# Performance work log

Measured on AMD Instinct MI355X. Metric: run time of the kernel, lower is better.

The kernel has to match this reference:

```python
import jax, jax.numpy as jnp
import numpy as np

N = 100000
E = 3200000
IN_F = 256
OUT_F = 64
ALPHA = 0.2  # LeakyReLU negative slope


def setup_inputs() -> dict:
    key = jax.random.key(0)
    k1, k2, k3, k4 = jax.random.split(key, 4)
    adj = jax.random.randint(k1, (2, E), 0, N, dtype=jnp.int64)
    x = jax.random.normal(k2, (N, IN_F), dtype=jnp.float32)
    # xavier-normal-ish scales
    W_fc = jax.random.normal(k3, (OUT_F, IN_F), dtype=jnp.float32) * (1.414 * np.sqrt(2.0 / (IN_F + OUT_F)))
    b_fc = jnp.zeros((OUT_F,), dtype=jnp.float32)
    a = jax.random.normal(k4, (1, 2 * OUT_F), dtype=jnp.float32) * (1.414 * np.sqrt(2.0 / (1 + 2 * OUT_F)))
    return {"adj": adj, "x": x, "W_fc": W_fc, "b_fc": b_fc, "a": a}


def reference(adj, x, W_fc, b_fc, a):
    src = adj[0]  # [E]
    dst = adj[1]  # [E]
    h = x @ W_fc.T + b_fc                       # [N, OUT_F]
    a1, a2 = a[0, :OUT_F], a[0, OUT_F:]         # split of attention vector
    # e = leakyrelu(a . [h_src || h_dst]) computed without materializing concat
    s1 = h @ a1                                  # [N]
    s2 = h @ a2                                  # [N]
    e = s1[src] + s2[dst]                        # [E]
    e = jnp.where(e > 0, e, ALPHA * e)           # LeakyReLU
    # dgl edge_softmax: softmax over edges grouped by destination node
    m = jax.ops.segment_max(e, dst, num_segments=N)     # [N]
    ex = jnp.exp(e - m[dst])                             # [E]
    denom = jax.ops.segment_sum(ex, dst, num_segments=N) # [N]
    att = ex / denom[dst]                                # [E]
    # SparseTensor(row=src, col=dst, value=att) @ h -> out[src] += att * h[dst]
    h_prime = jax.ops.segment_sum(att[:, None] * h[dst], src, num_segments=N)  # [N, OUT_F]
    return jax.nn.elu(h_prime)  # concat=True branch
```

## Files before the change

### kernel.cpp

```cpp
#include <hip/hip_runtime.h>
#include <math.h>

#define N_NODES 100000
#define N_EDGES 3200000
#define IN_F 256
#define OUT_F 64
#define LRELU_ALPHA 0.2f
#define NBKT 782
#define CAP 4480

typedef unsigned short u16;
typedef __attribute__((ext_vector_type(8))) short short8;
typedef __attribute__((ext_vector_type(4))) float floatx4;

__device__ inline u16 f2bf(float f) {
  unsigned u = __float_as_uint(f);
  u += 0x7FFFu + ((u >> 16) & 1u);
  return (u16)(u >> 16);
}
__device__ inline float bf2f(u16 h) {
  return __uint_as_float(((unsigned)h) << 16);
}

__global__ __launch_bounds__(256) void k_prep(const float* __restrict__ W,
                                              u16* __restrict__ Wbf,
                                              int* __restrict__ sfill,
                                              int* __restrict__ dfill) {
  if (blockIdx.x < 64) {
    int i = blockIdx.x * 256 + threadIdx.x;
    Wbf[i] = f2bf(W[i]);
  } else {
    for (int i = threadIdx.x; i < NBKT; i += 256) {
      sfill[i] = 0;
      dfill[i] = 0;
    }
  }
}

__global__ __launch_bounds__(256) void k_linear(
    const float* __restrict__ x, const u16* __restrict__ Wbf,
    const float* __restrict__ b, const float* __restrict__ a,
    u16* __restrict__ hbf, float* __restrict__ s1, float* __restrict__ s2) {
  __shared__ u16 Wlds[64 * 264];

  const int t = threadIdx.x;
#pragma unroll
  for (int p = 0; p < 8; p++) {
    int c = p * 256 + t;
    int row = c >> 5;
    int kc = (c & 31) * 8;
    *(short8*)&Wlds[row * 264 + kc] = *(const short8*)&Wbf[row * 256 + kc];
  }
  __syncthreads();

  const int w = t >> 6;
  const int lane = t & 63;
  const int col = lane & 15;
  const int q = lane >> 4;
  const int m0 = blockIdx.x * 64 + w * 16;

  floatx4 acc[4];
#pragma unroll
  for (int nt = 0; nt < 4; nt++) acc[nt] = (floatx4){0.f, 0.f, 0.f, 0.f};

  int mrow = m0 + col;
  if (mrow > N_NODES - 1) mrow = N_NODES - 1;
  const float* xrow = x + (size_t)mrow * IN_F + q * 8;

#pragma unroll
  for (int kk = 0; kk < 8; kk++) {
    float4 f0 = *(const float4*)(xrow + kk * 32);
    float4 f1 = *(const float4*)(xrow + kk * 32 + 4);
    short8 af;
    af[0] = (short)f2bf(f0.x);
    af[1] = (short)f2bf(f0.y);
    af[2] = (short)f2bf(f0.z);
    af[3] = (short)f2bf(f0.w);
    af[4] = (short)f2bf(f1.x);
    af[5] = (short)f2bf(f1.y);
    af[6] = (short)f2bf(f1.z);
    af[7] = (short)f2bf(f1.w);
#pragma unroll
    for (int nt = 0; nt < 4; nt++) {
      short8 bfr = *(const short8*)&Wlds[(nt * 16 + col) * 264 + kk * 32 + q * 8];
      acc[nt] = __builtin_amdgcn_mfma_f32_16x16x32_bf16(af, bfr, acc[nt], 0, 0, 0);
    }
  }

  float bv[4], a1v[4], a2v[4];
#pragma unroll
  for (int nt = 0; nt < 4; nt++) {
    bv[nt] = b[nt * 16 + col];
    a1v[nt] = a[nt * 16 + col];
    a2v[nt] = a[OUT_F + nt * 16 + col];
  }
#pragma unroll
  for (int r = 0; r < 4; r++) {
    int node = m0 + q * 4 + r;
    float p1 = 0.f, p2 = 0.f;
#pragma unroll
    for (int nt = 0; nt < 4; nt++) {
      float hv = acc[nt][r] + bv[nt];
      if (node < N_NODES) hbf[(size_t)node * OUT_F + nt * 16 + col] = f2bf(hv);
      p1 = fmaf(hv, a1v[nt], p1);
      p2 = fmaf(hv, a2v[nt], p2);
    }
#pragma unroll
    for (int s = 1; s < 16; s <<= 1) {
      p1 += __shfl_xor(p1, s, 16);
      p2 += __shfl_xor(p2, s, 16);
    }
    if (col == 0 && node < N_NODES) {
      s1[node] = p1;
      s2[node] = p2;
    }
  }
}

#define EPT_P 8
__global__ __launch_bounds__(1024) void k_place(
    const int* __restrict__ src, const int* __restrict__ dst,
    const float* __restrict__ s1, const float* __restrict__ s2,
    int* __restrict__ sfill, int* __restrict__ dfill,
    float2* __restrict__ pairS, float2* __restrict__ pairD) {
  __shared__ int lcS[NBKT];
  __shared__ int lcD[NBKT];
  __shared__ int lbS[NBKT];
  __shared__ int lbD[NBKT];
  const int t = threadIdx.x;
  for (int i = t; i < NBKT; i += 1024) {
    lcS[i] = 0;
    lcD[i] = 0;
  }
  __syncthreads();

  int base = blockIdx.x * (1024 * EPT_P) + t;
  float ex[EPT_P];
  int pk[EPT_P];
  int bs[EPT_P];
#pragma unroll
  for (int j = 0; j < EPT_P; j++) {
    int e = base + j * 1024;
    if (e < N_EDGES) {
      int s = src[e];
      int d = dst[e];
      float v = s1[s] + s2[d];
      v = v > 0.f ? v : LRELU_ALPHA * v;
      ex[j] = __expf(v);
      pk[j] = d | ((s & 127) << 17);
      bs[j] = s >> 7;
      atomicAdd(&lcS[bs[j]], 1);
      atomicAdd(&lcD[d >> 7], 1);
    }
  }
  __syncthreads();
  for (int i = t; i < NBKT; i += 1024) {
    int c = lcS[i];
    if (c) lbS[i] = atomicAdd(&sfill[i], c);
    int c2 = lcD[i];
    if (c2) lbD[i] = atomicAdd(&dfill[i], c2);
  }
  __syncthreads();
  for (int i = t; i < NBKT; i += 1024) {
    lcS[i] = 0;
    lcD[i] = 0;
  }
  __syncthreads();
#pragma unroll
  for (int j = 0; j < EPT_P; j++) {
    int e = base + j * 1024;
    if (e < N_EDGES) {
      int d = pk[j] & 0x1FFFF;
      int r = atomicAdd(&lcS[bs[j]], 1);
      pairS[(size_t)bs[j] * CAP + lbS[bs[j]] + r] =
          make_float2(ex[j], __int_as_float(pk[j]));
      int bd = d >> 7;
      int r2 = atomicAdd(&lcD[bd], 1);
      pairD[(size_t)bd * CAP + lbD[bd] + r2] =
          make_float2(ex[j], __int_as_float(d & 127));
    }
  }
}

__global__ __launch_bounds__(256) void k_denom(const int* __restrict__ dfill,
                                               const float2* __restrict__ pairD,
                                               float* __restrict__ denom_r) {
  __shared__ float lacc[128];
  const int t = threadIdx.x;
  const int bkt = blockIdx.x;
  if (t < 128) lacc[t] = 0.f;
  __syncthreads();
  int beg = bkt * CAP;
  int end = beg + dfill[bkt];
  for (int i = beg + t; i < end; i += 256) {
    float2 p = pairD[i];
    atomicAdd(&lacc[__float_as_int(p.y)], p.x);
  }
  __syncthreads();
  if (t < 128) {
    int node = bkt * 128 + t;
    if (node < N_NODES) denom_r[node] = 1.0f / lacc[t];
  }
}

__global__ __launch_bounds__(256) void k_sort2(
    const int* __restrict__ sfill, const float2* __restrict__ pairS,
    const float* __restrict__ denom_r, float2* __restrict__ pairA,
    int2* __restrict__ rowbe) {
  __shared__ int lcnt[128];
  __shared__ int cursor[128];
  __shared__ int w0tot;
  const int t = threadIdx.x;
  const int bkt = blockIdx.x;
  if (t < 128) lcnt[t] = 0;
  __syncthreads();

  const int beg = bkt * CAP;
  const int end = beg + sfill[bkt];

  for (int i = beg + t; i < end; i += 256) {
    int pkv = __float_as_int(pairS[i].y);
    atomicAdd(&lcnt[(pkv >> 17) & 127], 1);
  }
  __syncthreads();

  const int lane = t & 63;
  int v = (t < 128) ? lcnt[t] : 0;
  int val = v;
#pragma unroll
  for (int ofs = 1; ofs < 64; ofs <<= 1) {
    int u = __shfl_up(val, ofs, 64);
    if (lane >= ofs) val += u;
  }
  if (t == 63) w0tot = val;
  __syncthreads();
  int excl = val - v + ((t >= 64 && t < 128) ? w0tot : 0);
  if (t < 128) {
    cursor[t] = beg + excl;
    int node = bkt * 128 + t;
    if (node < N_NODES) rowbe[node] = make_int2(beg + excl, beg + excl + v);
  }
  __syncthreads();

  for (int i = beg + t; i < end; i += 256) {
    float2 p = pairS[i];
    int pkv = __float_as_int(p.y);
    int sl = (pkv >> 17) & 127;
    int d = pkv & 0x1FFFF;
    float att = p.x * denom_r[d];
    int pos = atomicAdd(&cursor[sl], 1);
    pairA[pos] = make_float2(att, __int_as_float(d));
  }
}

__global__ __launch_bounds__(256) void k_aggregate(
    const int2* __restrict__ rowbe, const float2* __restrict__ pairA,
    const u16* __restrict__ hbf, float* __restrict__ out) {
  int wid = (blockIdx.x * 256 + threadIdx.x) >> 6;
  int lane = threadIdx.x & 63;
  int g = lane >> 4;
  int sl = lane & 15;
  int node = wid * 4 + g;
  int2 be = (node < N_NODES) ? rowbe[node] : make_int2(0, 0);
  float4 acc = make_float4(0.f, 0.f, 0.f, 0.f);
  int i = be.x;
  const int end = be.y;
  for (; i + 1 < end; i += 2) {
    float2 p0 = pairA[i];
    float2 p1 = pairA[i + 1];
    int d0 = __float_as_int(p0.y);
    int d1 = __float_as_int(p1.y);
    ushort4 q0 = *(const ushort4*)&hbf[(size_t)d0 * OUT_F + sl * 4];
    ushort4 q1 = *(const ushort4*)&hbf[(size_t)d1 * OUT_F + sl * 4];
    acc.x = fmaf(p0.x, bf2f(q0.x), acc.x);
    acc.y = fmaf(p0.x, bf2f(q0.y), acc.y);
    acc.z = fmaf(p0.x, bf2f(q0.z), acc.z);
    acc.w = fmaf(p0.x, bf2f(q0.w), acc.w);
    acc.x = fmaf(p1.x, bf2f(q1.x), acc.x);
    acc.y = fmaf(p1.x, bf2f(q1.y), acc.y);
    acc.z = fmaf(p1.x, bf2f(q1.z), acc.z);
    acc.w = fmaf(p1.x, bf2f(q1.w), acc.w);
  }
  if (i < end) {
    float2 p = pairA[i];
    int d = __float_as_int(p.y);
    ushort4 q = *(const ushort4*)&hbf[(size_t)d * OUT_F + sl * 4];
    acc.x = fmaf(p.x, bf2f(q.x), acc.x);
    acc.y = fmaf(p.x, bf2f(q.y), acc.y);
    acc.z = fmaf(p.x, bf2f(q.z), acc.z);
    acc.w = fmaf(p.x, bf2f(q.w), acc.w);
  }
  if (node < N_NODES) {
    float4 o;
    o.x = acc.x > 0.f ? acc.x : expm1f(acc.x);
    o.y = acc.y > 0.f ? acc.y : expm1f(acc.y);
    o.z = acc.z > 0.f ? acc.z : expm1f(acc.z);
    o.w = acc.w > 0.f ? acc.w : expm1f(acc.w);
    *(float4*)(out + (size_t)node * OUT_F + sl * 4) = o;
  }
}

extern "C" void kernel_launch(void* const* d_in, const int* in_sizes, int n_in,
                              void* d_out, int out_size, void* d_ws,
                              size_t ws_size, hipStream_t stream) {
  const int* adj = (const int*)d_in[0];
  const float* x = (const float*)d_in[1];
  const float* W = (const float*)d_in[2];
  const float* b = (const float*)d_in[3];
  const float* a = (const float*)d_in[4];
  float* out = (float*)d_out;

  float* ws = (float*)d_ws;
  float* s1v = ws;
  float* s2v = ws + 100000;
  float* denom_r = ws + 200000;
  int* sfill = (int*)(ws + 300000);
  int* dfill = (int*)(ws + 300800);
  int2* rowbe = (int2*)(ws + 301600);
  float2* pairS = (float2*)(ws + 501600);
  float2* pairD = (float2*)(ws + 7508320);
  u16* hbf = (u16*)(ws + 14515040);
  u16* Wbf = (u16*)(ws + 17715040);

  float2* pairA = pairD;

  const int* src = adj;
  const int* dst = adj + N_EDGES;

  k_prep<<<65, 256, 0, stream>>>(W, Wbf, sfill, dfill);
  k_linear<<<(N_NODES + 63) / 64, 256, 0, stream>>>(x, Wbf, b, a, hbf, s1v, s2v);
  k_place<<<(N_EDGES + 1024 * EPT_P - 1) / (1024 * EPT_P), 1024, 0, stream>>>(
      src, dst, s1v, s2v, sfill, dfill, pairS, pairD);
  k_denom<<<NBKT, 256, 0, stream>>>(dfill, pairD, denom_r);
  k_sort2<<<NBKT, 256, 0, stream>>>(sfill, pairS, denom_r, pairA, rowbe);
  k_aggregate<<<(N_NODES + 15) / 16, 256, 0, stream>>>(rowbe, pairA, hbf, out);
}
```

Before: 423.8 us.

## Decouple edge bucketing from scores, store packed ints, recompute exp in consumers

Edge placement no longer reads s1/s2 or computes exp. It writes only packed int indices (4 bytes per edge instead of 8) into the src and dst buckets, and it now runs before the linear kernel. The denominator and sort kernels recompute the LeakyReLU and exp from s1/s2, staging the local-node half in shared memory. This halves the bucket traffic and removes the dependency of placement on the GEMM, at the cost of extra random gathers of s1/s2 and duplicated exp work. EPT_P also rises to 32 with re-reading src/dst instead of holding them in registers, and pairA gets its own buffer instead of aliasing pairD.

```diff
diff --git a/kernel.cpp b/kernel.cpp
--- a/kernel.cpp
+++ b/kernel.cpp
@@ -33,6 +33,60 @@
     for (int i = threadIdx.x; i < NBKT; i += 256) {
       sfill[i] = 0;
       dfill[i] = 0;
+    }
+  }
+}
+
+#define EPT_P 32
+__global__ __launch_bounds__(1024) void k_place(
+    const int* __restrict__ src, const int* __restrict__ dst,
+    int* __restrict__ sfill, int* __restrict__ dfill,
+    int* __restrict__ packS, int* __restrict__ packD) {
+  __shared__ int lcS[NBKT];
+  __shared__ int lcD[NBKT];
+  __shared__ int lbS[NBKT];
+  __shared__ int lbD[NBKT];
+  const int t = threadIdx.x;
+  for (int i = t; i < NBKT; i += 1024) {
+    lcS[i] = 0;
+    lcD[i] = 0;
+  }
+  __syncthreads();
+
+  const int base = blockIdx.x * (1024 * EPT_P);
+#pragma unroll 4
+  for (int j = 0; j < EPT_P; j++) {
+    int e = base + j * 1024 + t;
+    if (e < N_EDGES) {
+      atomicAdd(&lcS[src[e] >> 7], 1);
+      atomicAdd(&lcD[dst[e] >> 7], 1);
+    }
+  }
+  __syncthreads();
+  for (int i = t; i < NBKT; i += 1024) {
+    int c = lcS[i];
+    if (c) lbS[i] = atomicAdd(&sfill[i], c);
+    int c2 = lcD[i];
+    if (c2) lbD[i] = atomicAdd(&dfill[i], c2);
+  }
+  __syncthreads();
+  for (int i = t; i < NBKT; i += 1024) {
+    lcS[i] = 0;
+    lcD[i] = 0;
+  }
+  __syncthreads();
+#pragma unroll 4
+  for (int j = 0; j < EPT_P; j++) {
+    int e = base + j * 1024 + t;
+    if (e < N_EDGES) {
+      int s = src[e];
+      int d = dst[e];
+      int bs = s >> 7;
+      int bd = d >> 7;
+      int r = atomicAdd(&lcS[bs], 1);
+      packS[(size_t)bs * CAP + lbS[bs] + r] = d | ((s & 127) << 17);
+      int r2 = atomicAdd(&lcD[bd], 1);
+      packD[(size_t)bd * CAP + lbD[bd] + r2] = s | ((d & 127) << 17);
     }
   }
 }
@@ -117,84 +171,30 @@
   }
 }
 
-#define EPT_P 8
-__global__ __launch_bounds__(1024) void k_place(
-    const int* __restrict__ src, const int* __restrict__ dst,
-    const float* __restrict__ s1, const float* __restrict__ s2,
-    int* __restrict__ sfill, int* __restrict__ dfill,
-    float2* __restrict__ pairS, float2* __restrict__ pairD) {
-  __shared__ int lcS[NBKT];
-  __shared__ int lcD[NBKT];
-  __shared__ int lbS[NBKT];
-  __shared__ int lbD[NBKT];
-  const int t = threadIdx.x;
-  for (int i = t; i < NBKT; i += 1024) {
-    lcS[i] = 0;
-    lcD[i] = 0;
-  }
-  __syncthreads();
-
-  int base = blockIdx.x * (1024 * EPT_P) + t;
-  float ex[EPT_P];
-  int pk[EPT_P];
-  int bs[EPT_P];
-#pragma unroll
-  for (int j = 0; j < EPT_P; j++) {
-    int e = base + j * 1024;
-    if (e < N_EDGES) {
-      int s = src[e];
-      int d = dst[e];
-      float v = s1[s] + s2[d];
-      v = v > 0.f ? v : LRELU_ALPHA * v;
-      ex[j] = __expf(v);
-      pk[j] = d | ((s & 127) << 17);
-      bs[j] = s >> 7;
-      atomicAdd(&lcS[bs[j]], 1);
-      atomicAdd(&lcD[d >> 7], 1);
-    }
-  }
-  __syncthreads();
-  for (int i = t; i < NBKT; i += 1024) {
-    int c = lcS[i];
-    if (c) lbS[i] = atomicAdd(&sfill[i], c);
-    int c2 = lcD[i];
-    if (c2) lbD[i] = atomicAdd(&dfill[i], c2);
-  }
-  __syncthreads();
-  for (int i = t; i < NBKT; i += 1024) {
-    lcS[i] = 0;
-    lcD[i] = 0;
-  }
-  __syncthreads();
-#pragma unroll
-  for (int j = 0; j < EPT_P; j++) {
-    int e = base + j * 1024;
-    if (e < N_EDGES) {
-      int d = pk[j] & 0x1FFFF;
-      int r = atomicAdd(&lcS[bs[j]], 1);
-      pairS[(size_t)bs[j] * CAP + lbS[bs[j]] + r] =
-          make_float2(ex[j], __int_as_float(pk[j]));
-      int bd = d >> 7;
-      int r2 = atomicAdd(&lcD[bd], 1);
-      pairD[(size_t)bd * CAP + lbD[bd] + r2] =
-          make_float2(ex[j], __int_as_float(d & 127));
-    }
-  }
-}
-
 __global__ __launch_bounds__(256) void k_denom(const int* __restrict__ dfill,
-                                               const float2* __restrict__ pairD,
+                                               const int* __restrict__ packD,
+                                               const float* __restrict__ s1,
+                                               const float* __restrict__ s2,
                                                float* __restrict__ denom_r) {
   __shared__ float lacc[128];
+  __shared__ float s2l[128];
   const int t = threadIdx.x;
   const int bkt = blockIdx.x;
-  if (t < 128) lacc[t] = 0.f;
+  if (t < 128) {
+    lacc[t] = 0.f;
+    int node = bkt * 128 + t;
+    s2l[t] = (node < N_NODES) ? s2[node] : 0.f;
+  }
   __syncthreads();
   int beg = bkt * CAP;
   int end = beg + dfill[bkt];
   for (int i = beg + t; i < end; i += 256) {
-    float2 p = pairD[i];
-    atomicAdd(&lacc[__float_as_int(p.y)], p.x);
+    int pk = packD[i];
+    int s = pk & 0x1FFFF;
+    int dl = pk >> 17;
+    float v = s1[s] + s2l[dl];
+    v = v > 0.f ? v : LRELU_ALPHA * v;
+    atomicAdd(&lacc[dl], __expf(v));
   }
   __syncthreads();
   if (t < 128) {
@@ -204,23 +204,28 @@
 }
 
 __global__ __launch_bounds__(256) void k_sort2(
-    const int* __restrict__ sfill, const float2* __restrict__ pairS,
+    const int* __restrict__ sfill, const int* __restrict__ packS,
+    const float* __restrict__ s1, const float* __restrict__ s2,
     const float* __restrict__ denom_r, float2* __restrict__ pairA,
     int2* __restrict__ rowbe) {
   __shared__ int lcnt[128];
   __shared__ int cursor[128];
+  __shared__ float s1l[128];
   __shared__ int w0tot;
   const int t = threadIdx.x;
   const int bkt = blockIdx.x;
-  if (t < 128) lcnt[t] = 0;
+  if (t < 128) {
+    lcnt[t] = 0;
+    int node = bkt * 128 + t;
+    s1l[t] = (node < N_NODES) ? s1[node] : 0.f;
+  }
   __syncthreads();
 
   const int beg = bkt * CAP;
   const int end = beg + sfill[bkt];
 
   for (int i = beg + t; i < end; i += 256) {
-    int pkv = __float_as_int(pairS[i].y);
-    atomicAdd(&lcnt[(pkv >> 17) & 127], 1);
+    atomicAdd(&lcnt[packS[i] >> 17], 1);
   }
   __syncthreads();
 
@@ -243,11 +248,12 @@
   __syncthreads();
 
   for (int i = beg + t; i < end; i += 256) {
-    float2 p = pairS[i];
-    int pkv = __float_as_int(p.y);
-    int sl = (pkv >> 17) & 127;
-    int d = pkv & 0x1FFFF;
-    float att = p.x * denom_r[d];
+    int pk = packS[i];
+    int sl = pk >> 17;
+    int d = pk & 0x1FFFF;
+    float ev = s1l[sl] + s2[d];
+    ev = ev > 0.f ? ev : LRELU_ALPHA * ev;
+    float att = __expf(ev) * denom_r[d];
     int pos = atomicAdd(&cursor[sl], 1);
     pairA[pos] = make_float2(att, __int_as_float(d));
   }
@@ -317,21 +323,21 @@
   int* sfill = (int*)(ws + 300000);
   int* dfill = (int*)(ws + 300800);
   int2* rowbe = (int2*)(ws + 301600);
-  float2* pairS = (float2*)(ws + 501600);
-  float2* pairD = (float2*)(ws + 7508320);
+  int* packS = (int*)(ws + 501600);
+  int* packD = (int*)(ws + 4004960);
+  float2* pairA = (float2*)(ws + 7508320);
   u16* hbf = (u16*)(ws + 14515040);
   u16* Wbf = (u16*)(ws + 17715040);
 
-  float2* pairA = pairD;
-
   const int* src = adj;
   const int* dst = adj + N_EDGES;
 
   k_prep<<<65, 256, 0, stream>>>(W, Wbf, sfill, dfill);
+  k_place<<<(N_EDGES + 1024 * EPT_P - 1) / (1024 * EPT_P), 1024, 0, stream>>>(
+      src, dst, sfill, dfill, packS, packD);
   k_linear<<<(N_NODES + 63) / 64, 256, 0, stream>>>(x, Wbf, b, a, hbf, s1v, s2v);
-  k_place<<<(N_EDGES + 1024 * EPT_P - 1) / (1024 * EPT_P), 1024, 0, stream>>>(
-      src, dst, s1v, s2v, sfill, dfill, pairS, pairD);
-  k_denom<<<NBKT, 256, 0, stream>>>(dfill, pairD, denom_r);
-  k_sort2<<<NBKT, 256, 0, stream>>>(sfill, pairS, denom_r, pairA, rowbe);
+  k_denom<<<NBKT, 256, 0, stream>>>(dfill, packD, s1v, s2v, denom_r);
+  k_sort2<<<NBKT, 256, 0, stream>>>(sfill, packS, s1v, s2v, denom_r, pairA,
+                                    rowbe);
   k_aggregate<<<(N_NODES + 15) / 16, 256, 0, stream>>>(rowbe, pairA, hbf, out);
 }
```

Result: slower. 439.4 us (+3.7%).
